# Optimization experiments

Hardware: AMD Instinct MI355X
Metric: run time of the kernel (lower is better)

The kernel has to match this reference:

```python
import jax, jax.numpy as jnp
import numpy as np

B, N_F, N_E = 2, 2048, 4096
FDIM, EDIM, HDIM, HEADS = 128, 128, 64, 4
NEG_INF = -1e9


def setup_inputs() -> dict:
    key = jax.random.key(0)
    ks = jax.random.split(key, 8)
    F0 = jax.random.normal(ks[0], (B, N_F, FDIM), dtype=jnp.float32)
    E0 = jax.random.normal(ks[1], (B, N_E, EDIM), dtype=jnp.float32)
    adj_fe = jax.random.randint(ks[2], (N_F, N_E), 0, 2, dtype=jnp.int32)
    adj_ef = jax.random.randint(ks[3], (N_E, N_F), 0, 2, dtype=jnp.int32)
    # per-head kernels stacked on a leading head axis (same math as the python list)
    sf = float(np.sqrt(6.0 / (FDIM + HDIM)))
    se = float(np.sqrt(6.0 / (EDIM + HDIM)))
    sa = float(np.sqrt(6.0 / (HDIM + 1)))
    Wf = jax.random.uniform(ks[4], (HEADS, FDIM, HDIM), jnp.float32, -sf, sf)
    We = jax.random.uniform(ks[5], (HEADS, EDIM, HDIM), jnp.float32, -se, se)
    a_fe = jax.random.uniform(ks[6], (HEADS, HDIM), jnp.float32, -sa, sa)
    a_ef = jax.random.uniform(ks[7], (HEADS, HDIM), jnp.float32, -sa, sa)
    return {"F0": F0, "E0": E0, "adj_fe": adj_fe, "adj_ef": adj_ef,
            "Wf": Wf, "We": We, "a_fe": a_fe, "a_ef": a_ef}


def _attention(h_src, h_dst, A, a):
    # h_src: [B,H,N,D], h_dst: [B,H,M,D], A: [N,M], a: [H,D]
    e_src = jnp.einsum('bhnd,hd->bhn', h_src, a)
    e_dst = jnp.einsum('bhmd,hd->bhm', h_dst, a)
    e = jax.nn.leaky_relu(e_src[..., :, None] + e_dst[..., None, :], negative_slope=0.2)
    e = jnp.where(A[None, None] > 0, e, NEG_INF)
    alpha = jax.nn.softmax(e, axis=-1)
    # dropout on h_dst is identity at inference (Keras default training=False)
    return jnp.einsum('bhnm,bhmd->bhnd', alpha, h_dst)


def reference(F0, E0, adj_fe, adj_ef, Wf, We, a_fe, a_ef):
    F1 = jnp.einsum('bnf,hfd->bhnd', F0, Wf)  # [B,H,N_F,D]
    E1 = jnp.einsum('bme,hed->bhmd', E0, We)  # [B,H,N_E,D]
    hp_fe = _attention(F1, E1, adj_fe, a_fe)  # [B,H,N_F,D]
    hp_ef = _attention(E1, F1, adj_ef, a_ef)  # [B,H,N_E,D]
    # concat heads on feature axis
    out_fe = jnp.transpose(hp_fe, (0, 2, 1, 3)).reshape(B, N_F, HEADS * HDIM)
    out_ef = jnp.transpose(hp_ef, (0, 2, 1, 3)).reshape(B, N_E, HEADS * HDIM)
    out_fe = jax.nn.softmax(out_fe, axis=-1)
    out_ef = jax.nn.relu(out_ef)
    return (out_fe, out_ef)
```

## Files before the change

### kernel.cpp

```cpp
#include <hip/hip_runtime.h>
#include <hip/hip_bf16.h>
#include <stdint.h>

#define B_  2
#define NF_ 2048
#define NE_ 4096
#define FD_ 128
#define HD_ 64
#define H_  4

#define LOG2E 1.44269504f
#define KH    8.65617025f

typedef unsigned long long u64;
typedef __attribute__((ext_vector_type(4))) float f32x4;
typedef __attribute__((ext_vector_type(8))) short bf16x8;
typedef __attribute__((ext_vector_type(4))) unsigned uint32x4;

__device__ __forceinline__ float wave_sum64(float v) {
  #pragma unroll
  for (int m = 32; m >= 1; m >>= 1) v += __shfl_xor(v, m, 64);
  return v;
}
__device__ __forceinline__ float wave_max64(float v) {
  #pragma unroll
  for (int m = 32; m >= 1; m >>= 1) v = fmaxf(v, __shfl_xor(v, m, 64));
  return v;
}
__device__ __forceinline__ unsigned short bf16rne(float x) {
  unsigned u = __float_as_uint(x);
  return (unsigned short)((u + 0x7FFFu + ((u >> 16) & 1u)) >> 16);
}

__global__ __launch_bounds__(256) void pre_kernel(
    const float* __restrict__ Wf, const float* __restrict__ We,
    const float* __restrict__ a_fe, const float* __restrict__ a_ef,
    __hip_bfloat16* __restrict__ Wfrag, float* __restrict__ Wa)
{
  const int lane = threadIdx.x & 63, wid = threadIdx.x >> 6;
  const int dir = blockIdx.x >> 2, h = blockIdx.x & 3;
  const int cl = lane & 15, kq = lane >> 4;
  const float* W = (dir ? We : Wf) + (size_t)h * FD_ * HD_;
  __hip_bfloat16* fb = Wfrag + (size_t)(dir * 4 + h) * 8192;
  #pragma unroll
  for (int db = 0; db < 4; ++db) {
    unsigned short u[8];
    #pragma unroll
    for (int j = 0; j < 8; ++j)
      u[j] = bf16rne(W[(wid * 32 + kq * 8 + j) * HD_ + db * 16 + cl]);
    uint4 pk;
    pk.x = u[0] | ((unsigned)u[1] << 16);
    pk.y = u[2] | ((unsigned)u[3] << 16);
    pk.z = u[4] | ((unsigned)u[5] << 16);
    pk.w = u[6] | ((unsigned)u[7] << 16);
    *(uint4*)(fb + ((size_t)(wid * 4 + db) * 64 + lane) * 8) = pk;
  }
  if (wid == 0) {
    const float* a1 = a_fe + h * HD_;
    const float* a2 = a_ef + h * HD_;
    float* wa = Wa + (size_t)(dir * 4 + h) * 256;
    #pragma unroll
    for (int rep = 0; rep < 2; ++rep) {
      const int f = lane + rep * 64;
      const float* wr = W + (size_t)f * HD_;
      float s1 = 0.f, s2 = 0.f;
      #pragma unroll 8
      for (int d = 0; d < HD_; ++d) {
        s1 = fmaf(wr[d], a1[d], s1);
        s2 = fmaf(wr[d], a2[d], s2);
      }
      wa[f] = s1 * LOG2E;
      wa[128 + f] = s2 * LOG2E;
    }
  }
}

template<int SWAP, int NN>
__device__ __forceinline__ void proj_mfma(
    const float* __restrict__ X0, const __hip_bfloat16* __restrict__ Wfrag,
    const float* __restrict__ Wa, __hip_bfloat16* __restrict__ Vp,
    float2* __restrict__ rowO, unsigned* __restrict__ colO,
    int job, float* __restrict__ ldsX )
{
  const int lane = threadIdx.x & 63;
  const int cl = lane & 15, kq = lane >> 4;
  const int nj = NN >> 4;
  const int nt = job & (nj - 1);
  const int bh = job / nj;
  const int n0 = nt * 16;
  const int h = bh & 3, b = bh >> 2;
  const float* x0 = X0 + ((size_t)b * NN + n0 + cl) * FD_ + kq * 8;
  const __hip_bfloat16* fb = Wfrag + (size_t)((SWAP ? 4 : 0) + h) * 8192;
  const float* wa = Wa + (size_t)((SWAP ? 4 : 0) + h) * 256 + kq * 8;

  bf16x8 wf[4][4];
  #pragma unroll
  for (int ks = 0; ks < 4; ++ks)
    #pragma unroll
    for (int db = 0; db < 4; ++db)
      wf[ks][db] = *(const bf16x8*)(fb + ((size_t)(ks * 4 + db) * 64 + lane) * 8);

  bf16x8 xf[4];
  float d1 = 0.f, d2 = 0.f;
  #pragma unroll
  for (int ks = 0; ks < 4; ++ks) {
    const f32x4 xa = *(const f32x4*)(x0 + ks * 32);
    const f32x4 xb = *(const f32x4*)(x0 + ks * 32 + 4);
    const f32x4 w1a = *(const f32x4*)(wa + ks * 32);
    const f32x4 w1b = *(const f32x4*)(wa + ks * 32 + 4);
    const f32x4 w2a = *(const f32x4*)(wa + 128 + ks * 32);
    const f32x4 w2b = *(const f32x4*)(wa + 128 + ks * 32 + 4);
    #pragma unroll
    for (int i = 0; i < 4; ++i) {
      d1 = fmaf(xa[i], w1a[i], fmaf(xb[i], w1b[i], d1));
      d2 = fmaf(xa[i], w2a[i], fmaf(xb[i], w2b[i], d2));
    }
    #pragma unroll
    for (int i = 0; i < 4; ++i) {
      xf[ks][i]     = (short)bf16rne(xa[i]);
      xf[ks][i + 4] = (short)bf16rne(xb[i]);
    }
  }
  d1 += __shfl_xor(d1, 16, 64); d1 += __shfl_xor(d1, 32, 64);
  d2 += __shfl_xor(d2, 16, 64); d2 += __shfl_xor(d2, 32, 64);

  f32x4 acc[4] = {};
  #pragma unroll
  for (int ks = 0; ks < 4; ++ks)
    #pragma unroll
    for (int db = 0; db < 4; ++db)
      acc[db] = __builtin_amdgcn_mfma_f32_16x16x32_bf16(wf[ks][db], xf[ks],
                                                        acc[db], 0, 0, 0);
  #pragma unroll
  for (int db = 0; db < 4; ++db)
    *(f32x4*)(ldsX + cl * 68 + db * 16 + kq * 4) = acc[db];
  const int mt = n0 >> 6;
  #pragma unroll
  for (int c = 0; c < 2; ++c) {
    const int nb = n0 + c * 8;
    const int ks2 = (nb >> 5) & 1, q2 = (nb >> 3) & 3;
    unsigned short u[8];
    #pragma unroll
    for (int j = 0; j < 8; ++j)
      u[j] = bf16rne(ldsX[(c * 8 + j) * 68 + lane]);
    uint4 pk;
    pk.x = u[0] | ((unsigned)u[1] << 16);
    pk.y = u[2] | ((unsigned)u[3] << 16);
    pk.z = u[4] | ((unsigned)u[5] << 16);
    pk.w = u[6] | ((unsigned)u[7] << 16);
    *(uint4*)(Vp + ((size_t)((mt * 8 + ks2 * 4 + (lane >> 4)) * 64
                             + q2 * 16 + (lane & 15))) * 8) = pk;
  }
  if (kq == 0) {
    const float rd = SWAP ? d2 : d1;
    const float cd = SWAP ? d1 : d2;
    float2 rp;
    rp.x = exp2f(rd - KH);
    rp.y = exp2f(0.2f * rd - KH);
    rowO[(size_t)bh * NN + n0 + cl] = rp;
    colO[(size_t)bh * NN + n0 + cl] =
        (unsigned)bf16rne(exp2f(cd - KH)) |
        ((unsigned)bf16rne(exp2f(0.2f * cd - KH)) << 16);
  }
}

__device__ __forceinline__ void bitpack_body(
    const int* __restrict__ adj_fe, const int* __restrict__ adj_ef,
    u64* __restrict__ btfe, u64* __restrict__ btef, int id)
{
  const int lane = threadIdx.x & 63;
  const int* adj; u64* bt; int N, M, mt, g;
  if (id < 8192) {
    adj = adj_fe; bt = btfe; N = NF_; M = NE_;
    mt = id >> 7; g = id & 127;
  } else {
    const int k = id - 8192;
    adj = adj_ef; bt = btef; N = NE_; M = NF_;
    mt = k >> 8; g = k & 255;
  }
  const int* base = adj + (size_t)(g * 16) * M + mt * 64 + lane;
  int v[16];
  #pragma unroll
  for (int r = 0; r < 16; ++r) v[r] = base[(size_t)r * M];
  u64 mine = 0;
  #pragma unroll
  for (int r = 0; r < 16; ++r) {
    u64 msk = __ballot(v[r] != 0);
    if (lane == r) mine = msk;
  }
  if (lane < 16) bt[(size_t)mt * N + g * 16 + lane] = mine;
}

__global__ __launch_bounds__(256) void prep_kernel(
    const float* __restrict__ F0, const float* __restrict__ E0,
    const int* __restrict__ adj_fe, const int* __restrict__ adj_ef,
    const __hip_bfloat16* __restrict__ Wfrag, const float* __restrict__ Wa,
    __hip_bfloat16* __restrict__ Ftl, __hip_bfloat16* __restrict__ Etl,
    float2* __restrict__ rowF, unsigned* __restrict__ colF,
    float2* __restrict__ rowE, unsigned* __restrict__ colE,
    u64* __restrict__ btfe, u64* __restrict__ btef)
{
  __shared__ __align__(16) float ldsX[4][16 * 68];
  const int blk = blockIdx.x;
  const int wid = threadIdx.x >> 6;
  if (blk < 4096) {
    bitpack_body(adj_fe, adj_ef, btfe, btef, blk * 4 + wid);
  } else {
    const int job = (blk - 4096) * 4 + wid;
    if (job < 1024) {
      const int bh = job >> 7;
      proj_mfma<0, NF_>(F0, Wfrag, Wa,
                        Ftl + (size_t)bh * 32 * 4096,
                        rowF, colF, job, ldsX[wid]);
    } else {
      const int j2 = job - 1024;
      const int bh = j2 >> 8;
      proj_mfma<1, NE_>(E0, Wfrag, Wa,
                        Etl + (size_t)bh * 64 * 4096,
                        rowE, colE, j2, ldsX[wid]);
    }
  }
}

template<int TQ, int NN>
__device__ __forceinline__ void attn_wave(
    const __hip_bfloat16* __restrict__ vpp, const unsigned* __restrict__ colp,
    const u64* __restrict__ bt, float Ea, float Ga,
    int n0, int mt0, int cl, int kq,
    f32x4 (&accT)[4], f32x4 &accS)
{
  const int lane = threadIdx.x & 63;
  bf16x8 ones;
  #pragma unroll
  for (int i = 0; i < 8; ++i) ones[i] = (short)0x3F80;

  const __hip_bfloat16* tb = vpp + (size_t)mt0 * 4096 + (size_t)lane * 8;
  const unsigned* cp = colp + mt0 * 64 + kq * 8;
  const u64* bp = bt + (size_t)mt0 * NN + n0 + cl;
  const int shk = kq * 8;

  #pragma unroll 1
  for (int t = 0; t < TQ; ++t) {
    const bf16x8 vf0 = *(const bf16x8*)(tb);
    const bf16x8 vf1 = *(const bf16x8*)(tb + 512);
    const bf16x8 vf2 = *(const bf16x8*)(tb + 1024);
    const bf16x8 vf3 = *(const bf16x8*)(tb + 1536);
    const bf16x8 vf4 = *(const bf16x8*)(tb + 2048);
    const bf16x8 vf5 = *(const bf16x8*)(tb + 2560);
    const bf16x8 vf6 = *(const bf16x8*)(tb + 3072);
    const bf16x8 vf7 = *(const bf16x8*)(tb + 3584);
    const uint32x4 cc0 = *(const uint32x4*)(cp);
    const uint32x4 cc1 = *(const uint32x4*)(cp + 4);
    const uint32x4 cc2 = *(const uint32x4*)(cp + 32);
    const uint32x4 cc3 = *(const uint32x4*)(cp + 36);
    const u64 s0 = (*bp) >> shk;
    tb += 4096; cp += 64; bp += NN;

    bf16x8 pf;
    unsigned mw;

#define PJ(CC, JB, J) {                                                   \
      const unsigned cv = (CC)[J];                                        \
      const float Eb = __uint_as_float(cv << 16);                         \
      const float Gb = __uint_as_float(cv & 0xffff0000u);                 \
      float e = fmaxf(Ea * Eb, Ga * Gb);          \
      const int sm = ((int)(mw << (31 - (JB + J)))) >> 31;                \
      e = __int_as_float(__float_as_int(e) & sm);                         \
      __hip_bfloat16 hb = __float2bfloat16(e);                            \
      pf[JB + J] = *(const short*)&hb;                                    \
    }

    mw = (unsigned)s0;
    PJ(cc0, 0, 0) PJ(cc0, 0, 1) PJ(cc0, 0, 2) PJ(cc0, 0, 3)
    PJ(cc1, 4, 0) PJ(cc1, 4, 1) PJ(cc1, 4, 2) PJ(cc1, 4, 3)
    accS = __builtin_amdgcn_mfma_f32_16x16x32_bf16(pf, ones, accS, 0, 0, 0);
    accT[0] = __builtin_amdgcn_mfma_f32_16x16x32_bf16(pf, vf0, accT[0], 0, 0, 0);
    accT[1] = __builtin_amdgcn_mfma_f32_16x16x32_bf16(pf, vf1, accT[1], 0, 0, 0);
    accT[2] = __builtin_amdgcn_mfma_f32_16x16x32_bf16(pf, vf2, accT[2], 0, 0, 0);
    accT[3] = __builtin_amdgcn_mfma_f32_16x16x32_bf16(pf, vf3, accT[3], 0, 0, 0);

    mw = (unsigned)(s0 >> 32);
    PJ(cc2, 0, 0) PJ(cc2, 0, 1) PJ(cc2, 0, 2) PJ(cc2, 0, 3)
    PJ(cc3, 4, 0) PJ(cc3, 4, 1) PJ(cc3, 4, 2) PJ(cc3, 4, 3)
    accS = __builtin_amdgcn_mfma_f32_16x16x32_bf16(pf, ones, accS, 0, 0, 0);
    accT[0] = __builtin_amdgcn_mfma_f32_16x16x32_bf16(pf, vf4, accT[0], 0, 0, 0);
    accT[1] = __builtin_amdgcn_mfma_f32_16x16x32_bf16(pf, vf5, accT[1], 0, 0, 0);
    accT[2] = __builtin_amdgcn_mfma_f32_16x16x32_bf16(pf, vf6, accT[2], 0, 0, 0);
    accT[3] = __builtin_amdgcn_mfma_f32_16x16x32_bf16(pf, vf7, accT[3], 0, 0, 0);
#undef PJ
  }
}

__global__ __launch_bounds__(256) void attn_kernel(
    const __hip_bfloat16* __restrict__ Ftl, const __hip_bfloat16* __restrict__ Etl,
    const float2* __restrict__ rowF, const unsigned* __restrict__ colF,
    const float2* __restrict__ rowE, const unsigned* __restrict__ colE,
    const u64* __restrict__ btfe, const u64* __restrict__ btef,
    float* __restrict__ out)
{
  __shared__ __align__(16) float ldsO[4 * 4 * 64 * 4];
  __shared__ float ldsS[4 * 16];

  const int lane = threadIdx.x & 63;
  const int wid  = threadIdx.x >> 6;
  const int cl = lane & 15, kq = lane >> 4;
  const int blk = blockIdx.x;

  int N, bh, n0;
  float* obase;
  bool relu;
  f32x4 accT[4] = {};
  f32x4 accS = {0.f, 0.f, 0.f, 0.f};

  if (blk < 1024) {
    bh = blk & 7;
    n0 = (blk >> 3) * 16;
    N = NF_;
    const float2 rp = rowF[(size_t)bh * NF_ + n0 + cl];
    attn_wave<16, NF_>(Etl + (size_t)bh * 64 * 4096, colE + (size_t)bh * NE_,
                       btfe, rp.x, rp.y, n0, wid * 16, cl, kq, accT, accS);
    obase = out; relu = false;
  } else {
    const int k2 = blk - 1024;
    bh = k2 & 7;
    n0 = (k2 >> 3) * 16;
    N = NE_;
    const float2 rp = rowE[(size_t)bh * NE_ + n0 + cl];
    attn_wave<8, NE_>(Ftl + (size_t)bh * 32 * 4096, colF + (size_t)bh * NF_,
                      btef, rp.x, rp.y, n0, wid * 8, cl, kq, accT, accS);
    obase = out + (size_t)B_ * NF_ * 256; relu = true;
  }

  #pragma unroll
  for (int db = 0; db < 4; ++db)
    *(f32x4*)&ldsO[((db * 4 + wid) * 64 + lane) * 4] = accT[db];
  if (cl == 0) {
    #pragma unroll
    for (int reg = 0; reg < 4; ++reg)
      ldsS[wid * 16 + kq * 4 + reg] = accS[reg];
  }
  __syncthreads();

  f32x4 osum = {0.f, 0.f, 0.f, 0.f};
  #pragma unroll
  for (int s = 0; s < 4; ++s)
    osum += *(const f32x4*)&ldsO[((wid * 4 + s) * 64 + lane) * 4];
  float stot[4];
  #pragma unroll
  for (int reg = 0; reg < 4; ++reg) {
    stot[reg] = 0.f;
    #pragma unroll
    for (int s = 0; s < 4; ++s) stot[reg] += ldsS[s * 16 + kq * 4 + reg];
  }
  const int b = bh >> 2, h = bh & 3;
  float* orow = obase + ((size_t)b * N + n0 + kq * 4) * 256 + h * HD_ + wid * 16 + cl;
  #pragma unroll
  for (int reg = 0; reg < 4; ++reg) {
    float v = osum[reg] / stot[reg];
    if (relu) v = fmaxf(v, 0.0f);
    orow[reg * 256] = v;
  }
}

__global__ __launch_bounds__(256) void softmax256_kernel(float* __restrict__ io)
{
  const int t = threadIdx.x;
  const int lane = t & 63, wid = t >> 6;
  float v = io[(long)blockIdx.x * 256 + t];
  __shared__ float red[8];
  float m = wave_max64(v);
  if (lane == 0) red[wid] = m;
  __syncthreads();
  m = fmaxf(fmaxf(red[0], red[1]), fmaxf(red[2], red[3]));
  float e = __expf(v - m);
  float s = wave_sum64(e);
  if (lane == 0) red[4 + wid] = s;
  __syncthreads();
  s = (red[4] + red[5]) + (red[6] + red[7]);
  io[(long)blockIdx.x * 256 + t] = e / s;
}

extern "C" void kernel_launch(void* const* d_in, const int* in_sizes, int n_in,
                              void* d_out, int out_size, void* d_ws, size_t ws_size,
                              hipStream_t stream)
{
  const float* F0   = (const float*)d_in[0];
  const float* E0   = (const float*)d_in[1];
  const int* adj_fe = (const int*)d_in[2];
  const int* adj_ef = (const int*)d_in[3];
  const float* Wf   = (const float*)d_in[4];
  const float* We   = (const float*)d_in[5];
  const float* a_fe = (const float*)d_in[6];
  const float* a_ef = (const float*)d_in[7];
  float* out = (float*)d_out;

  char* ws = (char*)d_ws;
  float2* rowF = (float2*)ws;
  float2* rowE = (float2*)(ws + 131072);
  unsigned* colF = (unsigned*)(ws + 131072 + 262144);
  unsigned* colE = (unsigned*)((char*)colF + 65536);
  u64* btfe = (u64*)((char*)colE + 131072);
  u64* btef = btfe + (size_t)NF_ * (NE_ / 64);
  __hip_bfloat16* Ftl = (__hip_bfloat16*)(btef + (size_t)NE_ * (NF_ / 64));
  __hip_bfloat16* Etl = Ftl + (size_t)8 * 32 * 4096;
  __hip_bfloat16* Wfrag = Etl + (size_t)8 * 64 * 4096;
  float* Wa = (float*)(Wfrag + (size_t)8 * 8192);

  pre_kernel<<<8, 256, 0, stream>>>(Wf, We, a_fe, a_ef, Wfrag, Wa);
  prep_kernel<<<4864, 256, 0, stream>>>(F0, E0, adj_fe, adj_ef, Wfrag, Wa,
                                        Ftl, Etl, rowF, colF, rowE, colE,
                                        btfe, btef);
  attn_kernel<<<3072, 256, 0, stream>>>(Ftl, Etl, rowF, colF, rowE, colE,
                                        btfe, btef, out);
  softmax256_kernel<<<B_ * NF_, 256, 0, stream>>>(out);
}
```

Measured before the change: 88.69 us.

## Share V tiles across waves via double-buffered LDS in attention kernel

The attention kernel changes its work split. Before, each block's four waves split the key dimension for one 16-row query tile and were combined through LDS. Now each wave owns its own 16 query rows, and all four waves share one V tile per step, staged cooperatively into a double-buffered LDS buffer with a register prefetch of the next tile. This removes the cross-wave reduction and cuts redundant global loads of V, so the grid shrinks from 3072 to 768 blocks. In exchange there is a __syncthreads every iteration, far fewer blocks for the GPU, and longer serial loops per wave.

```diff
diff --git a/kernel.cpp b/kernel.cpp
--- a/kernel.cpp
+++ b/kernel.cpp
@@ -80,7 +80,7 @@
     const float* __restrict__ X0, const __hip_bfloat16* __restrict__ Wfrag,
     const float* __restrict__ Wa, __hip_bfloat16* __restrict__ Vp,
     float2* __restrict__ rowO, unsigned* __restrict__ colO,
-    int job, float* __restrict__ ldsX )
+    int job, float* __restrict__ ldsX)
 {
   const int lane = threadIdx.x & 63;
   const int cl = lane & 15, kq = lane >> 4;
@@ -157,10 +157,10 @@
     float2 rp;
     rp.x = exp2f(rd - KH);
     rp.y = exp2f(0.2f * rd - KH);
-    rowO[(size_t)bh * NN + n0 + cl] = rp;
-    colO[(size_t)bh * NN + n0 + cl] =
-        (unsigned)bf16rne(exp2f(cd - KH)) |
-        ((unsigned)bf16rne(exp2f(0.2f * cd - KH)) << 16);
+    const size_t idxn = (size_t)bh * NN + n0 + cl;
+    rowO[idxn] = rp;
+    colO[idxn] = (unsigned)bf16rne(exp2f(cd - KH)) |
+                 ((unsigned)bf16rne(exp2f(0.2f * cd - KH)) << 16);
   }
 }
 
@@ -209,56 +209,68 @@
     const int job = (blk - 4096) * 4 + wid;
     if (job < 1024) {
       const int bh = job >> 7;
-      proj_mfma<0, NF_>(F0, Wfrag, Wa,
-                        Ftl + (size_t)bh * 32 * 4096,
+      proj_mfma<0, NF_>(F0, Wfrag, Wa, Ftl + (size_t)bh * 32 * 4096,
                         rowF, colF, job, ldsX[wid]);
     } else {
       const int j2 = job - 1024;
       const int bh = j2 >> 8;
-      proj_mfma<1, NE_>(E0, Wfrag, Wa,
-                        Etl + (size_t)bh * 64 * 4096,
+      proj_mfma<1, NE_>(E0, Wfrag, Wa, Etl + (size_t)bh * 64 * 4096,
                         rowE, colE, j2, ldsX[wid]);
     }
   }
 }
 
 template<int TQ, int NN>
-__device__ __forceinline__ void attn_wave(
-    const __hip_bfloat16* __restrict__ vpp, const unsigned* __restrict__ colp,
-    const u64* __restrict__ bt, float Ea, float Ga,
-    int n0, int mt0, int cl, int kq,
+__device__ __forceinline__ void attn_wave_lds(
+    const char* __restrict__ vtile, const unsigned* __restrict__ colp,
+    const u64* __restrict__ bt, float Ea, float Ga, int nrow16,
+    char* __restrict__ lds0, char* __restrict__ lds1,
+    int lane, int wid, int cl, int kq,
     f32x4 (&accT)[4], f32x4 &accS)
 {
-  const int lane = threadIdx.x & 63;
   bf16x8 ones;
   #pragma unroll
   for (int i = 0; i < 8; ++i) ones[i] = (short)0x3F80;
 
-  const __hip_bfloat16* tb = vpp + (size_t)mt0 * 4096 + (size_t)lane * 8;
-  const unsigned* cp = colp + mt0 * 64 + kq * 8;
-  const u64* bp = bt + (size_t)mt0 * NN + n0 + cl;
+  const unsigned* cp = colp + kq * 8;
+  const u64* bp = bt + nrow16 + cl;
   const int shk = kq * 8;
+  const int soff = wid * 2048 + lane * 16;
+  const char* gp = vtile + soff;
+
+  uint4 sr0, sr1;
+  sr0 = *(const uint4*)(gp);
+  sr1 = *(const uint4*)(gp + 1024);
+  *(uint4*)(lds0 + soff) = sr0;
+  *(uint4*)(lds0 + soff + 1024) = sr1;
+  __syncthreads();
 
   #pragma unroll 1
   for (int t = 0; t < TQ; ++t) {
-    const bf16x8 vf0 = *(const bf16x8*)(tb);
-    const bf16x8 vf1 = *(const bf16x8*)(tb + 512);
-    const bf16x8 vf2 = *(const bf16x8*)(tb + 1024);
-    const bf16x8 vf3 = *(const bf16x8*)(tb + 1536);
-    const bf16x8 vf4 = *(const bf16x8*)(tb + 2048);
-    const bf16x8 vf5 = *(const bf16x8*)(tb + 2560);
-    const bf16x8 vf6 = *(const bf16x8*)(tb + 3072);
-    const bf16x8 vf7 = *(const bf16x8*)(tb + 3584);
+    const char* cb = (t & 1) ? lds1 : lds0;
+    char* nb = (t & 1) ? lds0 : lds1;
+    if (t + 1 < TQ) {
+      const char* gn = gp + (size_t)(t + 1) * 8192;
+      sr0 = *(const uint4*)(gn);
+      sr1 = *(const uint4*)(gn + 1024);
+    }
     const uint32x4 cc0 = *(const uint32x4*)(cp);
     const uint32x4 cc1 = *(const uint32x4*)(cp + 4);
     const uint32x4 cc2 = *(const uint32x4*)(cp + 32);
     const uint32x4 cc3 = *(const uint32x4*)(cp + 36);
     const u64 s0 = (*bp) >> shk;
-    tb += 4096; cp += 64; bp += NN;
+    cp += 64; bp += NN;
+    const bf16x8 vf0 = *(const bf16x8*)(cb + lane * 16);
+    const bf16x8 vf1 = *(const bf16x8*)(cb + 1024 + lane * 16);
+    const bf16x8 vf2 = *(const bf16x8*)(cb + 2048 + lane * 16);
+    const bf16x8 vf3 = *(const bf16x8*)(cb + 3072 + lane * 16);
+    const bf16x8 vf4 = *(const bf16x8*)(cb + 4096 + lane * 16);
+    const bf16x8 vf5 = *(const bf16x8*)(cb + 5120 + lane * 16);
+    const bf16x8 vf6 = *(const bf16x8*)(cb + 6144 + lane * 16);
+    const bf16x8 vf7 = *(const bf16x8*)(cb + 7168 + lane * 16);
 
     bf16x8 pf;
     unsigned mw;
-
 #define PJ(CC, JB, J) {                                                   \
       const unsigned cv = (CC)[J];                                        \
       const float Eb = __uint_as_float(cv << 16);                         \
@@ -269,7 +281,6 @@
       __hip_bfloat16 hb = __float2bfloat16(e);                            \
       pf[JB + J] = *(const short*)&hb;                                    \
     }
-
     mw = (unsigned)s0;
     PJ(cc0, 0, 0) PJ(cc0, 0, 1) PJ(cc0, 0, 2) PJ(cc0, 0, 3)
     PJ(cc1, 4, 0) PJ(cc1, 4, 1) PJ(cc1, 4, 2) PJ(cc1, 4, 3)
@@ -278,7 +289,6 @@
     accT[1] = __builtin_amdgcn_mfma_f32_16x16x32_bf16(pf, vf1, accT[1], 0, 0, 0);
     accT[2] = __builtin_amdgcn_mfma_f32_16x16x32_bf16(pf, vf2, accT[2], 0, 0, 0);
     accT[3] = __builtin_amdgcn_mfma_f32_16x16x32_bf16(pf, vf3, accT[3], 0, 0, 0);
-
     mw = (unsigned)(s0 >> 32);
     PJ(cc2, 0, 0) PJ(cc2, 0, 1) PJ(cc2, 0, 2) PJ(cc2, 0, 3)
     PJ(cc3, 4, 0) PJ(cc3, 4, 1) PJ(cc3, 4, 2) PJ(cc3, 4, 3)
@@ -288,77 +298,69 @@
     accT[2] = __builtin_amdgcn_mfma_f32_16x16x32_bf16(pf, vf6, accT[2], 0, 0, 0);
     accT[3] = __builtin_amdgcn_mfma_f32_16x16x32_bf16(pf, vf7, accT[3], 0, 0, 0);
 #undef PJ
-  }
-}
-
-__global__ __launch_bounds__(256) void attn_kernel(
+    if (t + 1 < TQ) {
+      *(uint4*)(nb + soff) = sr0;
+      *(uint4*)(nb + soff + 1024) = sr1;
+    }
+    __syncthreads();
+  }
+}
+
+__global__ __launch_bounds__(256, 2) void attn_kernel(
     const __hip_bfloat16* __restrict__ Ftl, const __hip_bfloat16* __restrict__ Etl,
     const float2* __restrict__ rowF, const unsigned* __restrict__ colF,
     const float2* __restrict__ rowE, const unsigned* __restrict__ colE,
     const u64* __restrict__ btfe, const u64* __restrict__ btef,
     float* __restrict__ out)
 {
-  __shared__ __align__(16) float ldsO[4 * 4 * 64 * 4];
-  __shared__ float ldsS[4 * 16];
+  __shared__ __align__(16) char lbuf0[8192];
+  __shared__ __align__(16) char lbuf1[8192];
 
   const int lane = threadIdx.x & 63;
   const int wid  = threadIdx.x >> 6;
   const int cl = lane & 15, kq = lane >> 4;
   const int blk = blockIdx.x;
 
-  int N, bh, n0;
+  int N, bh, nrow16;
   float* obase;
   bool relu;
   f32x4 accT[4] = {};
   f32x4 accS = {0.f, 0.f, 0.f, 0.f};
 
-  if (blk < 1024) {
+  if (blk < 256) {
     bh = blk & 7;
-    n0 = (blk >> 3) * 16;
+    nrow16 = (blk >> 3) * 64 + wid * 16;
     N = NF_;
-    const float2 rp = rowF[(size_t)bh * NF_ + n0 + cl];
-    attn_wave<16, NF_>(Etl + (size_t)bh * 64 * 4096, colE + (size_t)bh * NE_,
-                       btfe, rp.x, rp.y, n0, wid * 16, cl, kq, accT, accS);
+    const float2 rp = rowF[(size_t)bh * NF_ + nrow16 + cl];
+    attn_wave_lds<64, NF_>((const char*)(Etl + (size_t)bh * 64 * 4096),
+                           colE + (size_t)bh * NE_, btfe,
+                           rp.x, rp.y, nrow16, lbuf0, lbuf1,
+                           lane, wid, cl, kq, accT, accS);
     obase = out; relu = false;
   } else {
-    const int k2 = blk - 1024;
+    const int k2 = blk - 256;
     bh = k2 & 7;
-    n0 = (k2 >> 3) * 16;
+    nrow16 = (k2 >> 3) * 64 + wid * 16;
     N = NE_;
-    const float2 rp = rowE[(size_t)bh * NE_ + n0 + cl];
-    attn_wave<8, NE_>(Ftl + (size_t)bh * 32 * 4096, colF + (size_t)bh * NF_,
-                      btef, rp.x, rp.y, n0, wid * 8, cl, kq, accT, accS);
+    const float2 rp = rowE[(size_t)bh * NE_ + nrow16 + cl];
+    attn_wave_lds<32, NE_>((const char*)(Ftl + (size_t)bh * 32 * 4096),
+                           colF + (size_t)bh * NF_, btef,
+                           rp.x, rp.y, nrow16, lbuf0, lbuf1,
+                           lane, wid, cl, kq, accT, accS);
     obase = out + (size_t)B_ * NF_ * 256; relu = true;
   }
 
-  #pragma unroll
-  for (int db = 0; db < 4; ++db)
-    *(f32x4*)&ldsO[((db * 4 + wid) * 64 + lane) * 4] = accT[db];
-  if (cl == 0) {
-    #pragma unroll
-    for (int reg = 0; reg < 4; ++reg)
-      ldsS[wid * 16 + kq * 4 + reg] = accS[reg];
-  }
-  __syncthreads();
-
-  f32x4 osum = {0.f, 0.f, 0.f, 0.f};
-  #pragma unroll
-  for (int s = 0; s < 4; ++s)
-    osum += *(const f32x4*)&ldsO[((wid * 4 + s) * 64 + lane) * 4];
-  float stot[4];
+  const int b = bh >> 2, h = bh & 3;
+  float* orow = obase + ((size_t)b * N + nrow16 + kq * 4) * 256 + h * HD_ + cl;
   #pragma unroll
   for (int reg = 0; reg < 4; ++reg) {
-    stot[reg] = 0.f;
-    #pragma unroll
-    for (int s = 0; s < 4; ++s) stot[reg] += ldsS[s * 16 + kq * 4 + reg];
-  }
-  const int b = bh >> 2, h = bh & 3;
-  float* orow = obase + ((size_t)b * N + n0 + kq * 4) * 256 + h * HD_ + wid * 16 + cl;
-  #pragma unroll
-  for (int reg = 0; reg < 4; ++reg) {
-    float v = osum[reg] / stot[reg];
-    if (relu) v = fmaxf(v, 0.0f);
-    orow[reg * 256] = v;
+    const float inv = 1.0f / accS[reg];
+    #pragma unroll
+    for (int db = 0; db < 4; ++db) {
+      float v = accT[db][reg] * inv;
+      if (relu) v = fmaxf(v, 0.0f);
+      orow[reg * 256 + db * 16] = v;
+    }
   }
 }
 
@@ -396,10 +398,10 @@
 
   char* ws = (char*)d_ws;
   float2* rowF = (float2*)ws;
-  float2* rowE = (float2*)(ws + 131072);
-  unsigned* colF = (unsigned*)(ws + 131072 + 262144);
-  unsigned* colE = (unsigned*)((char*)colF + 65536);
-  u64* btfe = (u64*)((char*)colE + 131072);
+  float2* rowE = (float2*)(ws + (128 << 10));
+  unsigned* colF = (unsigned*)(ws + (384 << 10));
+  unsigned* colE = (unsigned*)(ws + (448 << 10));
+  u64* btfe = (u64*)(ws + (576 << 10));
   u64* btef = btfe + (size_t)NF_ * (NE_ / 64);
   __hip_bfloat16* Ftl = (__hip_bfloat16*)(btef + (size_t)NE_ * (NF_ / 64));
   __hip_bfloat16* Etl = Ftl + (size_t)8 * 32 * 4096;
@@ -410,7 +412,7 @@
   prep_kernel<<<4864, 256, 0, stream>>>(F0, E0, adj_fe, adj_ef, Wfrag, Wa,
                                         Ftl, Etl, rowF, colF, rowE, colE,
                                         btfe, btef);
-  attn_kernel<<<3072, 256, 0, stream>>>(Ftl, Etl, rowF, colF, rowE, colE,
-                                        btfe, btef, out);
+  attn_kernel<<<768, 256, 0, stream>>>(Ftl, Etl, rowF, colF, rowE, colE,
+                                       btfe, btef, out);
   softmax256_kernel<<<B_ * NF_, 256, 0, stream>>>(out);
 }
```

Result: slower. 96.21 us (+8.5%).
